# Kernel tuning notes

Hardware: AMD Instinct MI355X
Metric: run time of the kernel (lower is better)

Reference implementation:

```python
import jax, jax.numpy as jnp
import numpy as np

N = 8192
IN_F = 256
OUT_F = 256


def setup_inputs() -> dict:
    key = jax.random.key(0)
    k_v, k_adj, k1, k2, k3, kb = jax.random.split(key, 6)
    stdv = 1.0 / np.sqrt(OUT_F)
    V = jax.random.normal(k_v, (N, IN_F), dtype=jnp.float32)
    adj = jax.random.randint(k_adj, (N, N), 0, 4, dtype=jnp.int32)
    w1 = jax.random.uniform(k1, (IN_F, OUT_F), jnp.float32, -stdv, stdv)
    w2 = jax.random.uniform(k2, (IN_F, OUT_F), jnp.float32, -stdv, stdv)
    w3 = jax.random.uniform(k3, (IN_F, OUT_F), jnp.float32, -stdv, stdv)
    bias = jax.random.uniform(kb, (OUT_F,), jnp.float32, -stdv, stdv)
    return {"V": V, "adj": adj, "w1": w1, "w2": w2, "w3": w3, "bias": bias}


def reference(V, adj, w1, w2, w3, bias):
    # typed relational GCN: for each edge type k in {1,2,3},
    # aggregate (adj==k) @ (V @ wk), then sum and add bias
    o1 = jnp.matmul((adj == 1).astype(jnp.float32), jnp.matmul(V, w1))
    o2 = jnp.matmul((adj == 2).astype(jnp.float32), jnp.matmul(V, w2))
    o3 = jnp.matmul((adj == 3).astype(jnp.float32), jnp.matmul(V, w3))
    return o1 + o2 + o3 + bias
```

## Files before the change

kernel.cpp:

```cpp
#include <hip/hip_runtime.h>

typedef __attribute__((ext_vector_type(4))) float f32x4;
typedef __attribute__((ext_vector_type(16))) float f32x16;
typedef __attribute__((ext_vector_type(4))) unsigned short u16x4;
typedef __attribute__((ext_vector_type(4))) int i32x4;
typedef __attribute__((ext_vector_type(8))) __bf16 bf16x8;

union FragAB {
  u16x4 u[2];
  i32x4 v;
  bf16x8 f;
};

static __device__ __forceinline__ unsigned short f2bf(float x) {
  union { float f; unsigned u; } v;
  v.f = x;
  unsigned r = v.u + 0x7FFFu + ((v.u >> 16) & 1u);
  return (unsigned short)(r >> 16);
}

#define NN 8192

__global__ __launch_bounds__(256) void k_bias(const float* __restrict__ bias,
                                              float* __restrict__ out) {
  out[(size_t)blockIdx.x * 256 + threadIdx.x] = bias[threadIdx.x];
}

__global__ __launch_bounds__(256) void k_transform(
    const float* __restrict__ V, const float* __restrict__ w1,
    const float* __restrict__ w2, const float* __restrict__ w3,
    unsigned short* __restrict__ Bp) {
  int bx = blockIdx.x;
  int rb = bx & 63;
  int nb = bx >> 6;
  const float* W = (nb < 4) ? w1 : (nb < 8) ? w2 : w3;
  int nc0 = (nb & 3) * 64;
  int tid = threadIdx.x;
  int lane = tid & 63;
  int wv = tid >> 6;
  int wm = wv >> 1, wn = wv & 1;
  int q = lane >> 4, l16 = lane & 15;

  __shared__ unsigned short tA[128][36];
  __shared__ unsigned short tB[64][36];

  f32x4 acc[4][2];
#pragma unroll
  for (int i = 0; i < 4; i++)
#pragma unroll
    for (int j = 0; j < 2; j++) acc[i][j] = (f32x4)0.0f;

  for (int kk = 0; kk < 256; kk += 32) {
    {
      int r = tid >> 1, c0 = (tid & 1) * 16;
      const float* src = V + (size_t)(rb * 128 + r) * 256 + kk + c0;
      f32x4 f0 = *(const f32x4*)(src + 0);
      f32x4 f1 = *(const f32x4*)(src + 4);
      f32x4 f2 = *(const f32x4*)(src + 8);
      f32x4 f3 = *(const f32x4*)(src + 12);
      unsigned short* d = &tA[r][c0];
      d[0] = f2bf(f0.x);  d[1] = f2bf(f0.y);  d[2] = f2bf(f0.z);  d[3] = f2bf(f0.w);
      d[4] = f2bf(f1.x);  d[5] = f2bf(f1.y);  d[6] = f2bf(f1.z);  d[7] = f2bf(f1.w);
      d[8] = f2bf(f2.x);  d[9] = f2bf(f2.y);  d[10] = f2bf(f2.z); d[11] = f2bf(f2.w);
      d[12] = f2bf(f3.x); d[13] = f2bf(f3.y); d[14] = f2bf(f3.z); d[15] = f2bf(f3.w);
    }
    {
      int r = tid >> 3, c0 = (tid & 7) * 8;
      const float* src = W + (size_t)(kk + r) * 256 + nc0 + c0;
      f32x4 g0 = *(const f32x4*)(src);
      f32x4 g1 = *(const f32x4*)(src + 4);
      tB[c0 + 0][r] = f2bf(g0.x); tB[c0 + 1][r] = f2bf(g0.y);
      tB[c0 + 2][r] = f2bf(g0.z); tB[c0 + 3][r] = f2bf(g0.w);
      tB[c0 + 4][r] = f2bf(g1.x); tB[c0 + 5][r] = f2bf(g1.y);
      tB[c0 + 6][r] = f2bf(g1.z); tB[c0 + 7][r] = f2bf(g1.w);
    }
    __syncthreads();
    FragAB af[4], bf[2];
#pragma unroll
    for (int mt = 0; mt < 4; mt++) {
      const unsigned short* p = &tA[wm * 64 + mt * 16 + l16][q * 8];
      af[mt].u[0] = *(const u16x4*)p;
      af[mt].u[1] = *(const u16x4*)(p + 4);
    }
#pragma unroll
    for (int nt = 0; nt < 2; nt++) {
      const unsigned short* p = &tB[wn * 32 + nt * 16 + l16][q * 8];
      bf[nt].u[0] = *(const u16x4*)p;
      bf[nt].u[1] = *(const u16x4*)(p + 4);
    }
#pragma unroll
    for (int mt = 0; mt < 4; mt++)
#pragma unroll
      for (int nt = 0; nt < 2; nt++)
        acc[mt][nt] = __builtin_amdgcn_mfma_f32_16x16x32_bf16(
            af[mt].f, bf[nt].f, acc[mt][nt], 0, 0, 0);
    __syncthreads();
  }
  int ty = nb >> 2;
#pragma unroll
  for (int mt = 0; mt < 4; mt++)
#pragma unroll
    for (int nt = 0; nt < 2; nt++) {
      int n = (nb & 3) * 64 + wn * 32 + nt * 16 + l16;
      int j0 = rb * 128 + wm * 64 + mt * 16 + q * 4;
      u16x4 hv;
      hv.x = f2bf(acc[mt][nt].x);
      hv.y = f2bf(acc[mt][nt].y);
      hv.z = f2bf(acc[mt][nt].z);
      hv.w = f2bf(acc[mt][nt].w);
      size_t idx = (size_t)ty * 2097152 + (size_t)(j0 >> 4) * 4096 + n * 16 + (j0 & 15);
      *(u16x4*)(Bp + idx) = hv;
    }
}

__global__ __launch_bounds__(256) void k_agg(const int* __restrict__ adj,
                                             const unsigned short* __restrict__ Bp,
                                             float* __restrict__ out) {
  int bx = blockIdx.x;
  int ks = bx & 7, rb = bx >> 3;
  int tid = threadIdx.x, lane = tid & 63;
  int wn = tid >> 6;
  int q = lane >> 5, l32 = lane & 31;

  __shared__ unsigned short msk[2][3][64][36];

  f32x16 acc[2][2];
  acc[0][0] = (f32x16)0.0f;
  acc[0][1] = (f32x16)0.0f;
  acc[1][0] = (f32x16)0.0f;
  acc[1][1] = (f32x16)0.0f;

  int sr = tid >> 2, scg = tid & 3;
  const int* ap = adj + (size_t)(rb * 64 + sr) * NN + ks * 1024 + scg * 8;

  const unsigned short* bb[3][2];
#pragma unroll
  for (int ty = 0; ty < 3; ty++)
#pragma unroll
    for (int nt = 0; nt < 2; nt++) {
      int n = wn * 64 + nt * 32 + l32;
      bb[ty][nt] = Bp + (size_t)ty * 2097152 + (size_t)ks * 262144 + n * 16 + q * 8;
    }

  i32x4 a0 = *(const i32x4*)ap;
  i32x4 a1 = *(const i32x4*)(ap + 4);
  ap += 32;
  {
    int av[8] = {a0.x, a0.y, a0.z, a0.w, a1.x, a1.y, a1.z, a1.w};
#pragma unroll
    for (int ty = 0; ty < 3; ty++) {
      u16x4 lo, hi;
      lo.x = (av[0] == ty + 1) ? 0x3F80 : 0;
      lo.y = (av[1] == ty + 1) ? 0x3F80 : 0;
      lo.z = (av[2] == ty + 1) ? 0x3F80 : 0;
      lo.w = (av[3] == ty + 1) ? 0x3F80 : 0;
      hi.x = (av[4] == ty + 1) ? 0x3F80 : 0;
      hi.y = (av[5] == ty + 1) ? 0x3F80 : 0;
      hi.z = (av[6] == ty + 1) ? 0x3F80 : 0;
      hi.w = (av[7] == ty + 1) ? 0x3F80 : 0;
      unsigned short* d = &msk[0][ty][sr][scg * 8];
      *(u16x4*)d = lo;
      *(u16x4*)(d + 4) = hi;
    }
  }
  a0 = *(const i32x4*)ap;
  a1 = *(const i32x4*)(ap + 4);
  ap += 32;
  __syncthreads();

  for (int step = 0; step < 32; step++) {
    int buf = step & 1;
    FragAB bv[2][3][2];
    size_t soff = (size_t)step * 8192;
#pragma unroll
    for (int kh = 0; kh < 2; kh++)
#pragma unroll
      for (int ty = 0; ty < 3; ty++)
#pragma unroll
        for (int nt = 0; nt < 2; nt++)
          bv[kh][ty][nt].v = *(const i32x4*)(bb[ty][nt] + soff + kh * 4096);
    FragAB af[2][3][2];
#pragma unroll
    for (int kh = 0; kh < 2; kh++)
#pragma unroll
      for (int ty = 0; ty < 3; ty++)
#pragma unroll
        for (int mt = 0; mt < 2; mt++) {
          const unsigned short* p = &msk[buf][ty][mt * 32 + l32][kh * 16 + q * 8];
          af[kh][ty][mt].u[0] = *(const u16x4*)p;
          af[kh][ty][mt].u[1] = *(const u16x4*)(p + 4);
        }
#pragma unroll
    for (int kh = 0; kh < 2; kh++)
#pragma unroll
      for (int ty = 0; ty < 3; ty++) {
        acc[0][0] = __builtin_amdgcn_mfma_f32_32x32x16_bf16(
            af[kh][ty][0].f, bv[kh][ty][0].f, acc[0][0], 0, 0, 0);
        acc[0][1] = __builtin_amdgcn_mfma_f32_32x32x16_bf16(
            af[kh][ty][0].f, bv[kh][ty][1].f, acc[0][1], 0, 0, 0);
        acc[1][0] = __builtin_amdgcn_mfma_f32_32x32x16_bf16(
            af[kh][ty][1].f, bv[kh][ty][0].f, acc[1][0], 0, 0, 0);
        acc[1][1] = __builtin_amdgcn_mfma_f32_32x32x16_bf16(
            af[kh][ty][1].f, bv[kh][ty][1].f, acc[1][1], 0, 0, 0);
      }
    if (step < 31) {
      int av[8] = {a0.x, a0.y, a0.z, a0.w, a1.x, a1.y, a1.z, a1.w};
#pragma unroll
      for (int ty = 0; ty < 3; ty++) {
        u16x4 lo, hi;
        lo.x = (av[0] == ty + 1) ? 0x3F80 : 0;
        lo.y = (av[1] == ty + 1) ? 0x3F80 : 0;
        lo.z = (av[2] == ty + 1) ? 0x3F80 : 0;
        lo.w = (av[3] == ty + 1) ? 0x3F80 : 0;
        hi.x = (av[4] == ty + 1) ? 0x3F80 : 0;
        hi.y = (av[5] == ty + 1) ? 0x3F80 : 0;
        hi.z = (av[6] == ty + 1) ? 0x3F80 : 0;
        hi.w = (av[7] == ty + 1) ? 0x3F80 : 0;
        unsigned short* d = &msk[buf ^ 1][ty][sr][scg * 8];
        *(u16x4*)d = lo;
        *(u16x4*)(d + 4) = hi;
      }
      if (step < 30) {
        a0 = *(const i32x4*)ap;
        a1 = *(const i32x4*)(ap + 4);
        ap += 32;
      }
    }
    __syncthreads();
  }
#pragma unroll
  for (int mt = 0; mt < 2; mt++)
#pragma unroll
    for (int nt = 0; nt < 2; nt++) {
      int colbase = wn * 64 + nt * 32 + l32;
      int rowb = rb * 64 + mt * 32 + 4 * q;
#pragma unroll
      for (int r = 0; r < 16; r++) {
        int row = rowb + (r & 3) + 8 * (r >> 2);
        atomicAdd(out + (size_t)row * 256 + colbase, acc[mt][nt][r]);
      }
    }
}

extern "C" void kernel_launch(void* const* d_in, const int* in_sizes, int n_in,
                              void* d_out, int out_size, void* d_ws,
                              size_t ws_size, hipStream_t stream) {
  const float* V = (const float*)d_in[0];
  const int* adj = (const int*)d_in[1];
  const float* w1 = (const float*)d_in[2];
  const float* w2 = (const float*)d_in[3];
  const float* w3 = (const float*)d_in[4];
  const float* bias = (const float*)d_in[5];
  float* out = (float*)d_out;
  unsigned short* Bp = (unsigned short*)d_ws;

  k_bias<<<dim3(NN), dim3(256), 0, stream>>>(bias, out);
  k_transform<<<dim3(768), dim3(256), 0, stream>>>(V, w1, w2, w3, Bp);
  k_agg<<<dim3(1024), dim3(256), 0, stream>>>(adj, Bp, out);
}
```

Measured before the change: 489.0 us.

## Pack adjacency into 2-bit codes and build MFMA masks in registers

A new prep kernel reads the int32 adjacency once and packs it into 2-bit codes, 16 entries per word, while also writing the bias. The aggregation kernel now reads this 16x smaller packed matrix and builds bf16 one-hot A fragments directly in registers, dropping the shared-memory mask staging and the per-step barriers. It also retiles the work to 128x128 output blocks split across an N dimension. The price is an extra full pass over the 256 MB adjacency in the prep kernel, and the packed rows are now re-read by both N-blocks.

Result: slower. 533.1 us (+9.0%).

```diff
diff --git a/kernel.cpp b/kernel.cpp
--- a/kernel.cpp
+++ b/kernel.cpp
@@ -21,9 +21,31 @@
 
 #define NN 8192
 
-__global__ __launch_bounds__(256) void k_bias(const float* __restrict__ bias,
+__global__ __launch_bounds__(256) void k_prep(const int* __restrict__ adj,
+                                              const float* __restrict__ bias,
+                                              unsigned* __restrict__ adj2,
                                               float* __restrict__ out) {
-  out[(size_t)blockIdx.x * 256 + threadIdx.x] = bias[threadIdx.x];
+  int t = blockIdx.x * 256 + threadIdx.x;
+  int nT = gridDim.x * 256;
+  for (int g = t; g < 4194304; g += nT) {
+    const int* p = adj + (size_t)g * 16;
+    i32x4 a0 = *(const i32x4*)(p);
+    i32x4 a1 = *(const i32x4*)(p + 4);
+    i32x4 a2 = *(const i32x4*)(p + 8);
+    i32x4 a3 = *(const i32x4*)(p + 12);
+    unsigned w = (unsigned)(a0.x & 3)        | ((unsigned)(a0.y & 3) << 2)  |
+                 ((unsigned)(a0.z & 3) << 4) | ((unsigned)(a0.w & 3) << 6)  |
+                 ((unsigned)(a1.x & 3) << 8) | ((unsigned)(a1.y & 3) << 10) |
+                 ((unsigned)(a1.z & 3) << 12)| ((unsigned)(a1.w & 3) << 14) |
+                 ((unsigned)(a2.x & 3) << 16)| ((unsigned)(a2.y & 3) << 18) |
+                 ((unsigned)(a2.z & 3) << 20)| ((unsigned)(a2.w & 3) << 22) |
+                 ((unsigned)(a3.x & 3) << 24)| ((unsigned)(a3.y & 3) << 26) |
+                 ((unsigned)(a3.z & 3) << 28)| ((unsigned)(a3.w & 3) << 30);
+    adj2[g] = w;
+  }
+  for (int g = t; g < 524288; g += nT) {
+    *(f32x4*)(out + (size_t)g * 4) = *(const f32x4*)(bias + ((g * 4) & 255));
+  }
 }
 
 __global__ __launch_bounds__(256) void k_transform(
@@ -113,16 +135,16 @@
     }
 }
 
-__global__ __launch_bounds__(256) void k_agg(const int* __restrict__ adj,
-                                             const unsigned short* __restrict__ Bp,
-                                             float* __restrict__ out) {
+__global__ __launch_bounds__(256, 4) void k_agg(const unsigned* __restrict__ adj2,
+                                                const unsigned short* __restrict__ Bp,
+                                                float* __restrict__ out) {
   int bx = blockIdx.x;
-  int ks = bx & 7, rb = bx >> 3;
+  int ks = bx & 7, rb = (bx >> 3) & 63, nb = bx >> 9;
   int tid = threadIdx.x, lane = tid & 63;
-  int wn = tid >> 6;
+  int wv = tid >> 6;
+  int wm = wv >> 1, wn = wv & 1;
   int q = lane >> 5, l32 = lane & 31;
-
-  __shared__ unsigned short msk[2][3][64][36];
+  int qsh = q << 4;
 
   f32x16 acc[2][2];
   acc[0][0] = (f32x16)0.0f;
@@ -130,114 +152,68 @@
   acc[1][0] = (f32x16)0.0f;
   acc[1][1] = (f32x16)0.0f;
 
-  int sr = tid >> 2, scg = tid & 3;
-  const int* ap = adj + (size_t)(rb * 64 + sr) * NN + ks * 1024 + scg * 8;
-
-  const unsigned short* bb[3][2];
-#pragma unroll
-  for (int ty = 0; ty < 3; ty++)
+  const unsigned* ap0 = adj2 + (size_t)(rb * 128 + wm * 64 + l32) * 512 + ks * 64;
+  const unsigned* ap1 = ap0 + 32 * 512;
+
+  int n0 = nb * 128 + wn * 64 + l32;
+  const unsigned short* bp = Bp + (size_t)ks * 262144 + (size_t)n0 * 16 + q * 8;
+
+  unsigned long long c0 = *(const unsigned long long*)ap0;
+  unsigned long long c1 = *(const unsigned long long*)ap1;
+
+  for (int step = 0; step < 32; ++step) {
+    unsigned long long nx0 = 0, nx1 = 0;
+    if (step < 31) {
+      nx0 = *(const unsigned long long*)(ap0 + 2 * (step + 1));
+      nx1 = *(const unsigned long long*)(ap1 + 2 * (step + 1));
+    }
+#pragma unroll
+    for (int kh = 0; kh < 2; kh++) {
+      FragAB bv[3][2];
+#pragma unroll
+      for (int ty = 0; ty < 3; ty++)
+#pragma unroll
+        for (int nt = 0; nt < 2; nt++)
+          bv[ty][nt].v =
+              *(const i32x4*)(bp + (size_t)ty * 2097152 + kh * 4096 + nt * 512);
+      unsigned w0 = (unsigned)(kh ? (c0 >> 32) : c0) >> qsh;
+      unsigned w1 = (unsigned)(kh ? (c1 >> 32) : c1) >> qsh;
+#pragma unroll
+      for (int ty = 0; ty < 3; ty++) {
+        FragAB A0, A1;
+#pragma unroll
+        for (int d = 0; d < 4; d++) {
+          unsigned p00 = (w0 >> (4 * d)) & 3u, p01 = (w0 >> (4 * d + 2)) & 3u;
+          unsigned p10 = (w1 >> (4 * d)) & 3u, p11 = (w1 >> (4 * d + 2)) & 3u;
+          A0.v[d] = (int)((p00 == (unsigned)(ty + 1) ? 0x3F80u : 0u) |
+                          (p01 == (unsigned)(ty + 1) ? 0x3F800000u : 0u));
+          A1.v[d] = (int)((p10 == (unsigned)(ty + 1) ? 0x3F80u : 0u) |
+                          (p11 == (unsigned)(ty + 1) ? 0x3F800000u : 0u));
+        }
+        acc[0][0] = __builtin_amdgcn_mfma_f32_32x32x16_bf16(A0.f, bv[ty][0].f,
+                                                            acc[0][0], 0, 0, 0);
+        acc[0][1] = __builtin_amdgcn_mfma_f32_32x32x16_bf16(A0.f, bv[ty][1].f,
+                                                            acc[0][1], 0, 0, 0);
+        acc[1][0] = __builtin_amdgcn_mfma_f32_32x32x16_bf16(A1.f, bv[ty][0].f,
+                                                            acc[1][0], 0, 0, 0);
+        acc[1][1] = __builtin_amdgcn_mfma_f32_32x32x16_bf16(A1.f, bv[ty][1].f,
+                                                            acc[1][1], 0, 0, 0);
+      }
+    }
+    bp += 8192;
+    c0 = nx0;
+    c1 = nx1;
+  }
+#pragma unroll
+  for (int mt = 0; mt < 2; mt++)
 #pragma unroll
     for (int nt = 0; nt < 2; nt++) {
-      int n = wn * 64 + nt * 32 + l32;
-      bb[ty][nt] = Bp + (size_t)ty * 2097152 + (size_t)ks * 262144 + n * 16 + q * 8;
-    }
-
-  i32x4 a0 = *(const i32x4*)ap;
-  i32x4 a1 = *(const i32x4*)(ap + 4);
-  ap += 32;
-  {
-    int av[8] = {a0.x, a0.y, a0.z, a0.w, a1.x, a1.y, a1.z, a1.w};
-#pragma unroll
-    for (int ty = 0; ty < 3; ty++) {
-      u16x4 lo, hi;
-      lo.x = (av[0] == ty + 1) ? 0x3F80 : 0;
-      lo.y = (av[1] == ty + 1) ? 0x3F80 : 0;
-      lo.z = (av[2] == ty + 1) ? 0x3F80 : 0;
-      lo.w = (av[3] == ty + 1) ? 0x3F80 : 0;
-      hi.x = (av[4] == ty + 1) ? 0x3F80 : 0;
-      hi.y = (av[5] == ty + 1) ? 0x3F80 : 0;
-      hi.z = (av[6] == ty + 1) ? 0x3F80 : 0;
-      hi.w = (av[7] == ty + 1) ? 0x3F80 : 0;
-      unsigned short* d = &msk[0][ty][sr][scg * 8];
-      *(u16x4*)d = lo;
-      *(u16x4*)(d + 4) = hi;
-    }
-  }
-  a0 = *(const i32x4*)ap;
-  a1 = *(const i32x4*)(ap + 4);
-  ap += 32;
-  __syncthreads();
-
-  for (int step = 0; step < 32; step++) {
-    int buf = step & 1;
-    FragAB bv[2][3][2];
-    size_t soff = (size_t)step * 8192;
-#pragma unroll
-    for (int kh = 0; kh < 2; kh++)
-#pragma unroll
-      for (int ty = 0; ty < 3; ty++)
-#pragma unroll
-        for (int nt = 0; nt < 2; nt++)
-          bv[kh][ty][nt].v = *(const i32x4*)(bb[ty][nt] + soff + kh * 4096);
-    FragAB af[2][3][2];
-#pragma unroll
-    for (int kh = 0; kh < 2; kh++)
-#pragma unroll
-      for (int ty = 0; ty < 3; ty++)
-#pragma unroll
-        for (int mt = 0; mt < 2; mt++) {
-          const unsigned short* p = &msk[buf][ty][mt * 32 + l32][kh * 16 + q * 8];
-          af[kh][ty][mt].u[0] = *(const u16x4*)p;
-          af[kh][ty][mt].u[1] = *(const u16x4*)(p + 4);
-        }
-#pragma unroll
-    for (int kh = 0; kh < 2; kh++)
-#pragma unroll
-      for (int ty = 0; ty < 3; ty++) {
-        acc[0][0] = __builtin_amdgcn_mfma_f32_32x32x16_bf16(
-            af[kh][ty][0].f, bv[kh][ty][0].f, acc[0][0], 0, 0, 0);
-        acc[0][1] = __builtin_amdgcn_mfma_f32_32x32x16_bf16(
-            af[kh][ty][0].f, bv[kh][ty][1].f, acc[0][1], 0, 0, 0);
-        acc[1][0] = __builtin_amdgcn_mfma_f32_32x32x16_bf16(
-            af[kh][ty][1].f, bv[kh][ty][0].f, acc[1][0], 0, 0, 0);
-        acc[1][1] = __builtin_amdgcn_mfma_f32_32x32x16_bf16(
-            af[kh][ty][1].f, bv[kh][ty][1].f, acc[1][1], 0, 0, 0);
-      }
-    if (step < 31) {
-      int av[8] = {a0.x, a0.y, a0.z, a0.w, a1.x, a1.y, a1.z, a1.w};
-#pragma unroll
-      for (int ty = 0; ty < 3; ty++) {
-        u16x4 lo, hi;
-        lo.x = (av[0] == ty + 1) ? 0x3F80 : 0;
-        lo.y = (av[1] == ty + 1) ? 0x3F80 : 0;
-        lo.z = (av[2] == ty + 1) ? 0x3F80 : 0;
-        lo.w = (av[3] == ty + 1) ? 0x3F80 : 0;
-        hi.x = (av[4] == ty + 1) ? 0x3F80 : 0;
-        hi.y = (av[5] == ty + 1) ? 0x3F80 : 0;
-        hi.z = (av[6] == ty + 1) ? 0x3F80 : 0;
-        hi.w = (av[7] == ty + 1) ? 0x3F80 : 0;
-        unsigned short* d = &msk[buf ^ 1][ty][sr][scg * 8];
-        *(u16x4*)d = lo;
-        *(u16x4*)(d + 4) = hi;
-      }
-      if (step < 30) {
-        a0 = *(const i32x4*)ap;
-        a1 = *(const i32x4*)(ap + 4);
-        ap += 32;
-      }
-    }
-    __syncthreads();
-  }
-#pragma unroll
-  for (int mt = 0; mt < 2; mt++)
-#pragma unroll
-    for (int nt = 0; nt < 2; nt++) {
-      int colbase = wn * 64 + nt * 32 + l32;
-      int rowb = rb * 64 + mt * 32 + 4 * q;
+      int col = nb * 128 + wn * 64 + nt * 32 + l32;
+      int rowb = rb * 128 + wm * 64 + mt * 32 + 4 * q;
 #pragma unroll
       for (int r = 0; r < 16; r++) {
         int row = rowb + (r & 3) + 8 * (r >> 2);
-        atomicAdd(out + (size_t)row * 256 + colbase, acc[mt][nt][r]);
+        atomicAdd(out + (size_t)row * 256 + col, acc[mt][nt][r]);
       }
     }
 }
@@ -253,8 +229,9 @@
   const float* bias = (const float*)d_in[5];
   float* out = (float*)d_out;
   unsigned short* Bp = (unsigned short*)d_ws;
-
-  k_bias<<<dim3(NN), dim3(256), 0, stream>>>(bias, out);
+  unsigned* adj2 = (unsigned*)((char*)d_ws + 0xC00000);
+
+  k_prep<<<dim3(2048), dim3(256), 0, stream>>>(adj, bias, adj2, out);
   k_transform<<<dim3(768), dim3(256), 0, stream>>>(V, w1, w2, w3, Bp);
-  k_agg<<<dim3(1024), dim3(256), 0, stream>>>(adj, Bp, out);
-}
+  k_agg<<<dim3(1024), dim3(256), 0, stream>>>(adj2, Bp, out);
+}
```
